# Kernel optimization log

Hardware: AMD Instinct MI355X
Metric: run time of the kernel (lower is better)

## Reference

```python
import jax, jax.numpy as jnp
import numpy as np

N = 50000   # nodes
E = 800000  # edges (before self loops)
D_IN = 128
D_H = 128
C = 10
BN_EPS = 1e-5


def setup_inputs() -> dict:
    key = jax.random.key(0)
    ks = jax.random.split(key, 8)
    x = jax.random.normal(ks[0], (N, D_IN), dtype=jnp.float32)
    edge_index = jax.random.randint(ks[1], (2, E), 0, N, dtype=jnp.int32)
    s = 1.0 / np.sqrt(D_IN)  # ~xavier scale for square layers
    W1 = jax.random.normal(ks[2], (D_IN, D_H), dtype=jnp.float32) * s
    W2 = jax.random.normal(ks[3], (D_H, D_H), dtype=jnp.float32) * s
    W3 = jax.random.normal(ks[4], (D_H, D_H), dtype=jnp.float32) * s
    Wf = jax.random.normal(ks[5], (3 * D_H, C), dtype=jnp.float32) * (1.0 / np.sqrt(3 * D_H))
    zeros_h = jnp.zeros((D_H,), jnp.float32)
    ones_h = jnp.ones((D_H,), jnp.float32)
    return dict(
        x=x, edge_index=edge_index,
        W1=W1, b1=zeros_h, W2=W2, b2=zeros_h, W3=W3, b3=zeros_h,
        g1=ones_h, be1=zeros_h, g2=ones_h, be2=zeros_h, g3=ones_h, be3=zeros_h,
        Wf=Wf, bf=jnp.zeros((C,), jnp.float32),
    )


def _edges_with_norm(edge_index):
    # Add self loops, then symmetric GCN normalization: D^-1/2 (A+I) D^-1/2
    loop = jnp.arange(N, dtype=edge_index.dtype)
    row = jnp.concatenate([edge_index[0], loop])  # source
    col = jnp.concatenate([edge_index[1], loop])  # destination
    deg = jax.ops.segment_sum(jnp.ones_like(col, jnp.float32), col, num_segments=N)
    dinv = jnp.where(deg > 0, jax.lax.rsqrt(deg), 0.0)
    norm = dinv[row] * dinv[col]  # [E+N]
    return row, col, norm


def _gcn_conv(h, W, b, row, col, norm):
    h = h @ W  # linear first (as in PyG GCNConv)
    msg = h[row] * norm[:, None]           # gather + scale, [E+N, D]
    agg = jax.ops.segment_sum(msg, col, num_segments=N)  # scatter-add
    return agg + b


def _bn(h, g, b):
    # training-mode batch norm over the node dim (biased variance, as torch)
    m = h.mean(axis=0)
    v = jnp.mean((h - m) ** 2, axis=0)
    return g * (h - m) * jax.lax.rsqrt(v + BN_EPS) + b


def reference(x, edge_index, W1, b1, W2, b2, W3, b3,
              g1, be1, g2, be2, g3, be3, Wf, bf):
    row, col, norm = _edges_with_norm(edge_index)
    h1 = jax.nn.relu(_bn(_gcn_conv(x, W1, b1, row, col, norm), g1, be1))
    h2 = jax.nn.relu(_bn(_gcn_conv(h1, W2, b2, row, col, norm), g2, be2))
    h3 = jax.nn.relu(_bn(_gcn_conv(h2, W3, b3, row, col, norm), g3, be3))
    cat = jnp.concatenate([h1, h2, h3], axis=1)  # [N, 3*D_H]
    # dropout in eval mode == identity; identity readout (node level)
    return cat @ Wf + bf
```

## Files before the change

kernel.cpp:

```cpp
#include <hip/hip_runtime.h>

#define N_NODES 50000
#define N_EDGES 800000
#define D 128
#define C_OUT 10
#define BN_EPS 1e-5f
#define CAP 64
#define MTILE 32
#define GEMM_GRID 1563
#define LINKB 782
#define AGG_BLOCKS 2048
#define NCOPY 32
#define CSTR 136

typedef unsigned int uint32;
typedef __attribute__((ext_vector_type(8))) short bf16x8;
typedef __attribute__((ext_vector_type(4))) float f32x4;

__device__ __forceinline__ float bf2f(unsigned int u16) {
    unsigned int x = u16 << 16;
    float f;
    __builtin_memcpy(&f, &x, 4);
    return f;
}
__device__ __forceinline__ unsigned int f2bf(float f) {
    unsigned int x;
    __builtin_memcpy(&x, &f, 4);
    unsigned int r = x + 0x7FFFu + ((x >> 16) & 1u);
    return r >> 16;
}
__device__ __forceinline__ uint32 pack_bf2(float a, float b) {
    return f2bf(a) | (f2bf(b) << 16);
}


__global__ void k_setup(const float* __restrict__ W1, const float* __restrict__ W2,
                        const float* __restrict__ W3, const float* __restrict__ Wf,
                        unsigned short* __restrict__ WT, unsigned short* __restrict__ WfT,
                        int* __restrict__ cntp, float* __restrict__ sums) {
    int b = blockIdx.x, tid = threadIdx.x;
    if (b < 192) {
        int idx = b * 256 + tid;
        int mat = idx >> 14, rem = idx & 16383;
        int n = rem >> 7, k = rem & 127;
        const float* W = (mat == 0) ? W1 : ((mat == 1) ? W2 : W3);
        WT[idx] = (unsigned short)f2bf(W[k * 128 + n]);
    } else if (b < 216) {
        int idx = (b - 192) * 256 + tid;
        if (idx < 6144) {
            int li = idx >> 11, rem = idx & 2047;
            int n = rem >> 7, k = rem & 127;
            WfT[idx] = (n < C_OUT) ? (unsigned short)f2bf(Wf[(li * 128 + k) * C_OUT + n]) : 0;
        }
    } else {
        int i = (b - 216) * 256 + tid;
        if (i < N_NODES) cntp[i << 4] = 0;
        if (i < 3 * NCOPY * 256) sums[i] = 0.0f;
    }
}


__global__ void k_dinv(const int* __restrict__ cntp, int* __restrict__ cnt,
                       float* __restrict__ dinv) {
    int i = blockIdx.x * blockDim.x + threadIdx.x;
    if (i >= N_NODES) return;
    int c = cntp[i << 4];
    cnt[i] = (c < CAP) ? c : CAP;
    dinv[i] = rsqrtf((float)(c + 1));
}


__global__ void k_bnfin(const float* __restrict__ sums, const float* __restrict__ g,
                        const float* __restrict__ be, float* __restrict__ st) {
    int t = threadIdx.x;
    float sm = 0.f, sq = 0.f;
    for (int c = 0; c < NCOPY; ++c) {
        sm += sums[c * 256 + t];
        sq += sums[c * 256 + 128 + t];
    }
    float mean = sm * (1.0f / N_NODES);
    float var = fmaxf(sq * (1.0f / N_NODES) - mean * mean, 0.f);
    float s = g[t] * rsqrtf(var + BN_EPS);
    st[t] = s;
    st[128 + t] = be[t] - mean * s;
}


__global__ __launch_bounds__(128) void k_gemm(const float* __restrict__ Af32,
                                              const unsigned short* __restrict__ Abf,
                                              const unsigned short* __restrict__ WT,
                                              unsigned short* __restrict__ hl,
                                              const float* __restrict__ st,
                                              const unsigned short* __restrict__ WfT,
                                              const float* __restrict__ bfv,
                                              float* __restrict__ outp, int mode,
                                              const int* __restrict__ linkEi,
                                              int* __restrict__ cntp,
                                              int* __restrict__ adj) {
    __shared__ unsigned short SM[MTILE * CSTR];
    unsigned short* As = SM;
    int tid = threadIdx.x;
    int bid = blockIdx.x;

    if (linkEi && bid >= GEMM_GRID) {
        int lb = bid - GEMM_GRID;
        int d8[8], s8[8];
#pragma unroll
        for (int u = 0; u < 8; ++u) {
            int e = (lb * 8 + u) * 128 + tid;
            d8[u] = (e < N_EDGES) ? linkEi[N_EDGES + e] : -1;
            s8[u] = (e < N_EDGES) ? linkEi[e] : 0;
        }
#pragma unroll
        for (int u = 0; u < 8; ++u) {
            if (d8[u] >= 0) {
                int slot = atomicAdd(&cntp[d8[u] << 4], 1);
                if (slot < CAP) adj[(d8[u] << 6) + slot] = s8[u];
            }
        }
        return;
    }
    int row0 = bid * MTILE;

    if (Abf) {
        int c8 = tid & 15, cc = c8 * 8;
        float s8[8], t8[8];
        {
            float4 a0 = *(const float4*)&st[cc];
            float4 a1 = *(const float4*)&st[cc + 4];
            float4 b0 = *(const float4*)&st[128 + cc];
            float4 b1 = *(const float4*)&st[128 + cc + 4];
            s8[0] = a0.x; s8[1] = a0.y; s8[2] = a0.z; s8[3] = a0.w;
            s8[4] = a1.x; s8[5] = a1.y; s8[6] = a1.z; s8[7] = a1.w;
            t8[0] = b0.x; t8[1] = b0.y; t8[2] = b0.z; t8[3] = b0.w;
            t8[4] = b1.x; t8[5] = b1.y; t8[6] = b1.z; t8[7] = b1.w;
        }
        const uint4* H4 = (const uint4*)Abf;
#pragma unroll
        for (int i = 0; i < 4; ++i) {
            int idx = i * 128 + tid;
            int r = idx >> 4;
            int gr = row0 + r;
            uint4 v = make_uint4(0, 0, 0, 0);
            if (gr < N_NODES) v = H4[(size_t)gr * 16 + c8];
            uint32 w[4] = {v.x, v.y, v.z, v.w};
            uint32 o[4];
#pragma unroll
            for (int p = 0; p < 4; ++p) {
                float f0 = bf2f(w[p] & 0xFFFFu) * s8[2 * p] + t8[2 * p];
                float f1 = bf2f(w[p] >> 16) * s8[2 * p + 1] + t8[2 * p + 1];
                o[p] = pack_bf2(fmaxf(f0, 0.f), fmaxf(f1, 0.f));
            }
            int swz = c8 ^ (r & 15);
            *(uint4*)&As[r * 128 + swz * 8] = make_uint4(o[0], o[1], o[2], o[3]);
        }
    } else {
        const float4* A4 = (const float4*)Af32;
        int c4 = tid & 31;
#pragma unroll
        for (int i = 0; i < 8; ++i) {
            int idx = i * 128 + tid;
            int r = idx >> 5;
            int gr = row0 + r;
            float4 v = make_float4(0.f, 0.f, 0.f, 0.f);
            if (gr < N_NODES) v = A4[(size_t)gr * 32 + c4];
            ushort4 o;
            o.x = (unsigned short)f2bf(v.x);
            o.y = (unsigned short)f2bf(v.y);
            o.z = (unsigned short)f2bf(v.z);
            o.w = (unsigned short)f2bf(v.w);
            int swz = (c4 >> 1) ^ (r & 15);
            *(ushort4*)&As[r * 128 + swz * 8 + (c4 & 1) * 4] = o;
        }
    }
    __syncthreads();

    int wave = tid >> 6, lane = tid & 63;
    int quad = lane >> 4, l16 = lane & 15;
    int m0 = wave * 16;
    int m = m0 + l16;

    bf16x8 af[4];
#pragma unroll
    for (int ks = 0; ks < 4; ++ks) {
        int swz = (ks * 4 + quad) ^ (m & 15);
        af[ks] = *(bf16x8*)&As[m * 128 + swz * 8];
    }

    f32x4 acc[8];
#pragma unroll
    for (int nt = 0; nt < 8; ++nt) acc[nt] = (f32x4){0.f, 0.f, 0.f, 0.f};

#pragma unroll
    for (int nt = 0; nt < 8; ++nt) {
        int n = nt * 16 + l16;
        bf16x8 bfr[4];
#pragma unroll
        for (int ks = 0; ks < 4; ++ks)
            bfr[ks] = *(const bf16x8*)&WT[n * 128 + (ks * 4 + quad) * 8];
#pragma unroll
        for (int ks = 0; ks < 4; ++ks)
            acc[nt] = __builtin_amdgcn_mfma_f32_16x16x32_bf16(af[ks], bfr[ks], acc[nt], 0, 0, 0);
    }

    if (mode != 0) {
        f32x4 accO = (f32x4){0.f, 0.f, 0.f, 0.f};
#pragma unroll
        for (int ks = 0; ks < 4; ++ks) {
            bf16x8 bw = *(const bf16x8*)&WfT[l16 * 128 + (ks * 4 + quad) * 8];
            accO = __builtin_amdgcn_mfma_f32_16x16x32_bf16(af[ks], bw, accO, 0, 0, 0);
        }
        if (l16 < C_OUT) {
#pragma unroll
            for (int reg = 0; reg < 4; ++reg) {
                int gm = row0 + m0 + quad * 4 + reg;
                if (gm < N_NODES) {
                    size_t o = (size_t)gm * C_OUT + l16;
                    float v = accO[reg];
                    if (mode == 1) outp[o] = v + bfv[l16];
                    else outp[o] += v;
                }
            }
        }
    }

    __syncthreads();
#pragma unroll
    for (int reg = 0; reg < 4; ++reg) {
        int lm = m0 + quad * 4 + reg;
#pragma unroll
        for (int nt = 0; nt < 8; ++nt)
            SM[lm * CSTR + nt * 16 + l16] = (unsigned short)f2bf(acc[nt][reg]);
    }
    __syncthreads();
    uint4* H4o = (uint4*)hl;
#pragma unroll
    for (int i = 0; i < 4; ++i) {
        int idx = i * 128 + tid;
        int r = idx >> 4, c8 = idx & 15;
        int gr = row0 + r;
        if (gr < N_NODES)
            H4o[(size_t)gr * 16 + c8] = *(uint4*)&SM[r * CSTR + c8 * 8];
    }
}


__global__ __launch_bounds__(256) void k_agg(const unsigned short* __restrict__ hl,
                                             const int* __restrict__ adj,
                                             const int* __restrict__ cnt,
                                             const float* __restrict__ dinv,
                                             unsigned short* __restrict__ agg,
                                             float* __restrict__ sums) {
    __shared__ float red[4][256];
    int tid = threadIdx.x;
    int lane = tid & 63;
    int gw = (blockIdx.x << 2) | (tid >> 6);
    float sx = 0.f, qx = 0.f, sy = 0.f, qy = 0.f;

    for (int node = gw; node < N_NODES; node += AGG_BLOCKS * 4) {
        const int* row = adj + ((size_t)node << 6);
        int n = cnt[node];
        float di = dinv[node];
        uint32 ps = *(const uint32*)&hl[(size_t)node * 128 + lane * 2];
        float ax = bf2f(ps & 0xFFFFu) * di;
        float ay = bf2f(ps >> 16) * di;
        int e = 0;
        for (; e + 7 < n; e += 8) {
            int j[8];
#pragma unroll
            for (int u = 0; u < 8; ++u) j[u] = row[e + u];
            float w[8];
            uint32 p[8];
#pragma unroll
            for (int u = 0; u < 8; ++u) {
                w[u] = dinv[j[u]];
                p[u] = *(const uint32*)&hl[(size_t)j[u] * 128 + lane * 2];
            }
#pragma unroll
            for (int u = 0; u < 8; ++u) {
                ax += bf2f(p[u] & 0xFFFFu) * w[u];
                ay += bf2f(p[u] >> 16) * w[u];
            }
        }
        for (; e < n; ++e) {
            int j = row[e];
            float w = dinv[j];
            uint32 p = *(const uint32*)&hl[(size_t)j * 128 + lane * 2];
            ax += bf2f(p & 0xFFFFu) * w;
            ay += bf2f(p >> 16) * w;
        }
        float ox = ax * di, oy = ay * di;
        *(uint32*)&agg[(size_t)node * 128 + lane * 2] = pack_bf2(ox, oy);
        sx += ox; qx += ox * ox; sy += oy; qy += oy * oy;
    }

    red[0][tid] = sx; red[1][tid] = qx; red[2][tid] = sy; red[3][tid] = qy;
    __syncthreads();
    int s = tid >> 6, l = tid & 63;
    float v = red[s][l] + red[s][64 + l] + red[s][128 + l] + red[s][192 + l];
    atomicAdd(&sums[((blockIdx.x & (NCOPY - 1)) << 8) + (s & 1) * 128 + 2 * l + (s >> 1)], v);
}


__global__ __launch_bounds__(128) void k_out_mfma(const unsigned short* __restrict__ h,
                                                  const unsigned short* __restrict__ WfT,
                                                  float* __restrict__ outp,
                                                  const float* __restrict__ st) {
    __shared__ unsigned short As[MTILE * 128];
    int tid = threadIdx.x;
    int row0 = blockIdx.x * MTILE;

    int c8 = tid & 15, cc = c8 * 8;
    float s8[8], t8[8];
    {
        float4 a0 = *(const float4*)&st[cc];
        float4 a1 = *(const float4*)&st[cc + 4];
        float4 b0 = *(const float4*)&st[128 + cc];
        float4 b1 = *(const float4*)&st[128 + cc + 4];
        s8[0] = a0.x; s8[1] = a0.y; s8[2] = a0.z; s8[3] = a0.w;
        s8[4] = a1.x; s8[5] = a1.y; s8[6] = a1.z; s8[7] = a1.w;
        t8[0] = b0.x; t8[1] = b0.y; t8[2] = b0.z; t8[3] = b0.w;
        t8[4] = b1.x; t8[5] = b1.y; t8[6] = b1.z; t8[7] = b1.w;
    }
    const uint4* H4 = (const uint4*)h;
#pragma unroll
    for (int i = 0; i < 4; ++i) {
        int idx = i * 128 + tid;
        int r = idx >> 4;
        int gr = row0 + r;
        uint4 v = make_uint4(0, 0, 0, 0);
        if (gr < N_NODES) v = H4[(size_t)gr * 16 + c8];
        uint32 w[4] = {v.x, v.y, v.z, v.w};
        uint32 o[4];
#pragma unroll
        for (int p = 0; p < 4; ++p) {
            float f0 = bf2f(w[p] & 0xFFFFu) * s8[2 * p] + t8[2 * p];
            float f1 = bf2f(w[p] >> 16) * s8[2 * p + 1] + t8[2 * p + 1];
            o[p] = pack_bf2(fmaxf(f0, 0.f), fmaxf(f1, 0.f));
        }
        int swz = c8 ^ (r & 15);
        *(uint4*)&As[r * 128 + swz * 8] = make_uint4(o[0], o[1], o[2], o[3]);
    }
    __syncthreads();

    int wave = tid >> 6, lane = tid & 63;
    int quad = lane >> 4, l16 = lane & 15;
    int m0 = wave * 16;
    int m = m0 + l16;

    f32x4 accO = (f32x4){0.f, 0.f, 0.f, 0.f};
#pragma unroll
    for (int ks = 0; ks < 4; ++ks) {
        bf16x8 bw = *(const bf16x8*)&WfT[l16 * 128 + (ks * 4 + quad) * 8];
        int swz = (ks * 4 + quad) ^ (m & 15);
        bf16x8 av = *(bf16x8*)&As[m * 128 + swz * 8];
        accO = __builtin_amdgcn_mfma_f32_16x16x32_bf16(av, bw, accO, 0, 0, 0);
    }
    if (l16 < C_OUT) {
#pragma unroll
        for (int reg = 0; reg < 4; ++reg) {
            int gm = row0 + m0 + quad * 4 + reg;
            if (gm < N_NODES)
                outp[(size_t)gm * C_OUT + l16] += accO[reg];
        }
    }
}


extern "C" void kernel_launch(void* const* d_in, const int* in_sizes, int n_in,
                              void* d_out, int out_size, void* d_ws, size_t ws_size,
                              hipStream_t stream) {
    const float* x  = (const float*)d_in[0];
    const int*   ei = (const int*)d_in[1];
    const float* W1 = (const float*)d_in[2];
    const float* W2 = (const float*)d_in[4];
    const float* W3 = (const float*)d_in[6];
    const float* g1  = (const float*)d_in[8];
    const float* be1 = (const float*)d_in[9];
    const float* g2  = (const float*)d_in[10];
    const float* be2 = (const float*)d_in[11];
    const float* g3  = (const float*)d_in[12];
    const float* be3 = (const float*)d_in[13];
    const float* Wf  = (const float*)d_in[14];
    const float* bf  = (const float*)d_in[15];
    float* out = (float*)d_out;

    char* ws = (char*)d_ws;
    size_t off = 0;
    auto alloc = [&](size_t bytes) -> void* {
        void* p = ws + off;
        off = (off + bytes + 255) & ~(size_t)255;
        return p;
    };
    int*   cntp  = (int*)alloc((size_t)N_NODES * 16 * 4);
    int*   adj   = (int*)alloc((size_t)N_NODES * CAP * 4);
    int*   cnt   = (int*)alloc((size_t)N_NODES * 4);
    float* dinv  = (float*)alloc((size_t)N_NODES * 4);
    float* sums  = (float*)alloc((size_t)3 * NCOPY * 256 * 4);
    float* st    = (float*)alloc((size_t)3 * 256 * 4);
    unsigned short* WT   = (unsigned short*)alloc((size_t)3 * 128 * 128 * 2);
    unsigned short* WfT  = (unsigned short*)alloc((size_t)3 * 16 * 128 * 2);
    unsigned short* hl   = (unsigned short*)alloc((size_t)N_NODES * 128 * 2);
    unsigned short* bufA = (unsigned short*)alloc((size_t)N_NODES * 128 * 2);
    unsigned short* bufB = (unsigned short*)alloc((size_t)N_NODES * 128 * 2);

    const int TPB = 256;
    const int SL = NCOPY * 256;
    k_setup<<<412, 256, 0, stream>>>(W1, W2, W3, Wf, WT, WfT, cntp, sums);

    k_gemm<<<GEMM_GRID + LINKB, 128, 0, stream>>>(
        x, nullptr, WT, hl, nullptr, nullptr,
        nullptr, nullptr, 0, ei, cntp, adj);
    k_dinv<<<(N_NODES + TPB - 1) / TPB, TPB, 0, stream>>>(cntp, cnt, dinv);
    k_agg<<<AGG_BLOCKS, 256, 0, stream>>>(hl, adj, cnt, dinv, bufA, sums + 0);
    k_bnfin<<<1, 128, 0, stream>>>(sums + 0, g1, be1, st + 0);

    k_gemm<<<GEMM_GRID, 128, 0, stream>>>(nullptr, bufA, WT + 16384, hl, st + 0,
                                          WfT, bf, out, 1, nullptr, nullptr, nullptr);
    k_agg<<<AGG_BLOCKS, 256, 0, stream>>>(hl, adj, cnt, dinv, bufB, sums + SL);
    k_bnfin<<<1, 128, 0, stream>>>(sums + SL, g2, be2, st + 256);

    k_gemm<<<GEMM_GRID, 128, 0, stream>>>(nullptr, bufB, WT + 32768, hl, st + 256,
                                          WfT + 2048, nullptr, out, 2, nullptr, nullptr, nullptr);
    k_agg<<<AGG_BLOCKS, 256, 0, stream>>>(hl, adj, cnt, dinv, bufA, sums + 2 * SL);
    k_bnfin<<<1, 128, 0, stream>>>(sums + 2 * SL, g3, be3, st + 512);

    k_out_mfma<<<GEMM_GRID, 128, 0, stream>>>(bufA, WfT + 4096, out, st + 512);
}
```

Baseline: 330.9 us.

## Fuse BN finalize into aggregation and prescale GEMM output by dinv

The separate single-block BN finalize kernel is removed. The last aggregation block to finish, found with an atomic done counter, now computes the scale and shift. For layers 2 and 3 the GEMM epilogue multiplies each output row by its source dinv, so the aggregation skips the per-neighbor dinv gather and multiply. This removes three kernel launches and one random gather per edge, in exchange for a last-block reduction with a threadfence and slightly different bf16 rounding.

```diff
diff --git a/kernel.cpp b/kernel.cpp
--- a/kernel.cpp
+++ b/kernel.cpp
@@ -37,7 +37,8 @@
 __global__ void k_setup(const float* __restrict__ W1, const float* __restrict__ W2,
                         const float* __restrict__ W3, const float* __restrict__ Wf,
                         unsigned short* __restrict__ WT, unsigned short* __restrict__ WfT,
-                        int* __restrict__ cntp, float* __restrict__ sums) {
+                        int* __restrict__ cntp, float* __restrict__ sums,
+                        int* __restrict__ done) {
     int b = blockIdx.x, tid = threadIdx.x;
     if (b < 192) {
         int idx = b * 256 + tid;
@@ -56,6 +57,7 @@
         int i = (b - 216) * 256 + tid;
         if (i < N_NODES) cntp[i << 4] = 0;
         if (i < 3 * NCOPY * 256) sums[i] = 0.0f;
+        if (i < 3) done[i] = 0;
     }
 }
 
@@ -67,22 +69,6 @@
     int c = cntp[i << 4];
     cnt[i] = (c < CAP) ? c : CAP;
     dinv[i] = rsqrtf((float)(c + 1));
-}
-
-
-__global__ void k_bnfin(const float* __restrict__ sums, const float* __restrict__ g,
-                        const float* __restrict__ be, float* __restrict__ st) {
-    int t = threadIdx.x;
-    float sm = 0.f, sq = 0.f;
-    for (int c = 0; c < NCOPY; ++c) {
-        sm += sums[c * 256 + t];
-        sq += sums[c * 256 + 128 + t];
-    }
-    float mean = sm * (1.0f / N_NODES);
-    float var = fmaxf(sq * (1.0f / N_NODES) - mean * mean, 0.f);
-    float s = g[t] * rsqrtf(var + BN_EPS);
-    st[t] = s;
-    st[128 + t] = be[t] - mean * s;
 }
 
 
@@ -94,6 +80,7 @@
                                               const unsigned short* __restrict__ WfT,
                                               const float* __restrict__ bfv,
                                               float* __restrict__ outp, int mode,
+                                              const float* __restrict__ dinvp,
                                               const int* __restrict__ linkEi,
                                               int* __restrict__ cntp,
                                               int* __restrict__ adj) {
@@ -224,13 +211,22 @@
         }
     }
 
+    float dv[4] = {1.f, 1.f, 1.f, 1.f};
+    if (dinvp) {
+#pragma unroll
+        for (int reg = 0; reg < 4; ++reg) {
+            int gm = row0 + m0 + quad * 4 + reg;
+            dv[reg] = (gm < N_NODES) ? dinvp[gm] : 0.f;
+        }
+    }
+
     __syncthreads();
 #pragma unroll
     for (int reg = 0; reg < 4; ++reg) {
         int lm = m0 + quad * 4 + reg;
 #pragma unroll
         for (int nt = 0; nt < 8; ++nt)
-            SM[lm * CSTR + nt * 16 + l16] = (unsigned short)f2bf(acc[nt][reg]);
+            SM[lm * CSTR + nt * 16 + l16] = (unsigned short)f2bf(acc[nt][reg] * dv[reg]);
     }
     __syncthreads();
     uint4* H4o = (uint4*)hl;
@@ -250,8 +246,14 @@
                                              const int* __restrict__ cnt,
                                              const float* __restrict__ dinv,
                                              unsigned short* __restrict__ agg,
-                                             float* __restrict__ sums) {
+                                             float* __restrict__ sums,
+                                             const float* __restrict__ g,
+                                             const float* __restrict__ be,
+                                             float* __restrict__ st,
+                                             int* __restrict__ done,
+                                             int scaled) {
     __shared__ float red[4][256];
+    __shared__ int lastFlag;
     int tid = threadIdx.x;
     int lane = tid & 63;
     int gw = (blockIdx.x << 2) | (tid >> 6);
@@ -262,32 +264,51 @@
         int n = cnt[node];
         float di = dinv[node];
         uint32 ps = *(const uint32*)&hl[(size_t)node * 128 + lane * 2];
-        float ax = bf2f(ps & 0xFFFFu) * di;
-        float ay = bf2f(ps >> 16) * di;
+        float ax, ay;
+        if (scaled) {
+            ax = bf2f(ps & 0xFFFFu);
+            ay = bf2f(ps >> 16);
+        } else {
+            ax = bf2f(ps & 0xFFFFu) * di;
+            ay = bf2f(ps >> 16) * di;
+        }
         int e = 0;
         for (; e + 7 < n; e += 8) {
             int j[8];
 #pragma unroll
             for (int u = 0; u < 8; ++u) j[u] = row[e + u];
-            float w[8];
             uint32 p[8];
 #pragma unroll
-            for (int u = 0; u < 8; ++u) {
-                w[u] = dinv[j[u]];
+            for (int u = 0; u < 8; ++u)
                 p[u] = *(const uint32*)&hl[(size_t)j[u] * 128 + lane * 2];
-            }
-#pragma unroll
-            for (int u = 0; u < 8; ++u) {
-                ax += bf2f(p[u] & 0xFFFFu) * w[u];
-                ay += bf2f(p[u] >> 16) * w[u];
+            if (scaled) {
+#pragma unroll
+                for (int u = 0; u < 8; ++u) {
+                    ax += bf2f(p[u] & 0xFFFFu);
+                    ay += bf2f(p[u] >> 16);
+                }
+            } else {
+                float w[8];
+#pragma unroll
+                for (int u = 0; u < 8; ++u) w[u] = dinv[j[u]];
+#pragma unroll
+                for (int u = 0; u < 8; ++u) {
+                    ax += bf2f(p[u] & 0xFFFFu) * w[u];
+                    ay += bf2f(p[u] >> 16) * w[u];
+                }
             }
         }
         for (; e < n; ++e) {
             int j = row[e];
-            float w = dinv[j];
             uint32 p = *(const uint32*)&hl[(size_t)j * 128 + lane * 2];
-            ax += bf2f(p & 0xFFFFu) * w;
-            ay += bf2f(p >> 16) * w;
+            if (scaled) {
+                ax += bf2f(p & 0xFFFFu);
+                ay += bf2f(p >> 16);
+            } else {
+                float w = dinv[j];
+                ax += bf2f(p & 0xFFFFu) * w;
+                ay += bf2f(p >> 16) * w;
+            }
         }
         float ox = ax * di, oy = ay * di;
         *(uint32*)&agg[(size_t)node * 128 + lane * 2] = pack_bf2(ox, oy);
@@ -299,6 +320,25 @@
     int s = tid >> 6, l = tid & 63;
     float v = red[s][l] + red[s][64 + l] + red[s][128 + l] + red[s][192 + l];
     atomicAdd(&sums[((blockIdx.x & (NCOPY - 1)) << 8) + (s & 1) * 128 + 2 * l + (s >> 1)], v);
+
+    __syncthreads();
+    if (tid == 0) lastFlag = (atomicAdd(done, 1) == AGG_BLOCKS - 1) ? 1 : 0;
+    __syncthreads();
+    if (lastFlag) {
+        __threadfence();
+        if (tid < 128) {
+            float sm = 0.f, sq = 0.f;
+            for (int c = 0; c < NCOPY; ++c) {
+                sm += sums[c * 256 + tid];
+                sq += sums[c * 256 + 128 + tid];
+            }
+            float mean = sm * (1.0f / N_NODES);
+            float var = fmaxf(sq * (1.0f / N_NODES) - mean * mean, 0.f);
+            float sc = g[tid] * rsqrtf(var + BN_EPS);
+            st[tid] = sc;
+            st[128 + tid] = be[tid] - mean * sc;
+        }
+    }
 }
 
 
@@ -398,6 +438,7 @@
     float* dinv  = (float*)alloc((size_t)N_NODES * 4);
     float* sums  = (float*)alloc((size_t)3 * NCOPY * 256 * 4);
     float* st    = (float*)alloc((size_t)3 * 256 * 4);
+    int*   done  = (int*)alloc(3 * 4);
     unsigned short* WT   = (unsigned short*)alloc((size_t)3 * 128 * 128 * 2);
     unsigned short* WfT  = (unsigned short*)alloc((size_t)3 * 16 * 128 * 2);
     unsigned short* hl   = (unsigned short*)alloc((size_t)N_NODES * 128 * 2);
@@ -406,24 +447,25 @@
 
     const int TPB = 256;
     const int SL = NCOPY * 256;
-    k_setup<<<412, 256, 0, stream>>>(W1, W2, W3, Wf, WT, WfT, cntp, sums);
+    k_setup<<<412, 256, 0, stream>>>(W1, W2, W3, Wf, WT, WfT, cntp, sums, done);
 
     k_gemm<<<GEMM_GRID + LINKB, 128, 0, stream>>>(
         x, nullptr, WT, hl, nullptr, nullptr,
-        nullptr, nullptr, 0, ei, cntp, adj);
+        nullptr, nullptr, 0, nullptr, ei, cntp, adj);
     k_dinv<<<(N_NODES + TPB - 1) / TPB, TPB, 0, stream>>>(cntp, cnt, dinv);
-    k_agg<<<AGG_BLOCKS, 256, 0, stream>>>(hl, adj, cnt, dinv, bufA, sums + 0);
-    k_bnfin<<<1, 128, 0, stream>>>(sums + 0, g1, be1, st + 0);
+    k_agg<<<AGG_BLOCKS, 256, 0, stream>>>(hl, adj, cnt, dinv, bufA, sums + 0,
+                                          g1, be1, st + 0, done + 0, 0);
 
     k_gemm<<<GEMM_GRID, 128, 0, stream>>>(nullptr, bufA, WT + 16384, hl, st + 0,
-                                          WfT, bf, out, 1, nullptr, nullptr, nullptr);
-    k_agg<<<AGG_BLOCKS, 256, 0, stream>>>(hl, adj, cnt, dinv, bufB, sums + SL);
-    k_bnfin<<<1, 128, 0, stream>>>(sums + SL, g2, be2, st + 256);
+                                          WfT, bf, out, 1, dinv, nullptr, nullptr, nullptr);
+    k_agg<<<AGG_BLOCKS, 256, 0, stream>>>(hl, adj, cnt, dinv, bufB, sums + SL,
+                                          g2, be2, st + 256, done + 1, 1);
 
     k_gemm<<<GEMM_GRID, 128, 0, stream>>>(nullptr, bufB, WT + 32768, hl, st + 256,
-                                          WfT + 2048, nullptr, out, 2, nullptr, nullptr, nullptr);
-    k_agg<<<AGG_BLOCKS, 256, 0, stream>>>(hl, adj, cnt, dinv, bufA, sums + 2 * SL);
-    k_bnfin<<<1, 128, 0, stream>>>(sums + 2 * SL, g3, be3, st + 512);
+                                          WfT + 2048, nullptr, out, 2, dinv,
+                                          nullptr, nullptr, nullptr);
+    k_agg<<<AGG_BLOCKS, 256, 0, stream>>>(hl, adj, cnt, dinv, bufA, sums + 2 * SL,
+                                          g3, be3, st + 512, done + 2, 1);
 
     k_out_mfma<<<GEMM_GRID, 128, 0, stream>>>(bufA, WfT + 4096, out, st + 512);
 }
```

Result: slower. 424.2 us (+28.2%).
